# Kernel optimization log

Hardware: AMD Instinct MI355X
Metric: run time of the kernel (lower is better)

## Reference

```python
import jax, jax.numpy as jnp
import numpy as np

DRN = 0.4
TWO_PI = 2.0 * np.pi


def _mlp(x, ws, bs):
    # torch_geometric MLP with act='LeakyRelu' (slope 0.01), dropout=0 (eval), norm treated as identity (eval running stats)
    for w, b in zip(ws[:-1], bs[:-1]):
        x = jax.nn.leaky_relu(x @ w + b, 0.01)
    return x @ ws[-1] + bs[-1]


def _conv(x, ws, bs):
    # x: [B, N, F] = [pt, h..., ang_re, ang_im]. Dense masked equivalent of radius-graph EdgeConv.
    ang = x[..., -2:]
    d2 = jnp.sum((ang[:, :, None, :] - ang[:, None, :, :]) ** 2, -1)
    adj = (d2 <= DRN * DRN).astype(x.dtype)  # [B,N,N], i=target, j=source, self-loops included (radius ball)
    h = x[..., 1:-2]
    B, N, H = h.shape
    hi = jnp.broadcast_to(h[:, :, None, :], (B, N, N, H))
    hj = jnp.broadcast_to(h[:, None, :, :], (B, N, N, H))
    re, im = ang[..., 0], ang[..., 1]
    r2 = re * re + im * im
    nrm = jnp.maximum(jnp.sqrt(r2[:, :, None] * r2[:, None, :]), 1e-12)
    cos = (re[:, :, None] * re[:, None, :] + im[:, :, None] * im[:, None, :]) / nrm
    sin = (im[:, :, None] * re[:, None, :] - re[:, :, None] * im[:, None, :]) / nrm
    feat = jnp.concatenate([hi, hj, hj - hi, cos[..., None], sin[..., None]], -1)
    m = _mlp(feat, ws, bs)  # [B,N,N,H_out+1]
    # pt-weighted aggregation: message pt is the TARGET's pt (x_i[:, :1] in torch code)
    pt = x[..., 0]
    msg_pt = pt[:, :, None] * adj
    denom = jnp.sum(msg_pt, -1, keepdims=True)
    w = jnp.where(denom > 0, msg_pt / denom, 0.0)  # nan_to_num equivalent
    agg = jnp.einsum('bij,bijk->bik', w, m)
    sw = jnp.sum(w, -1)
    agg_pt = pt * sw                      # sum_j w * pt_i
    agg_ang = ang * sw[..., None]          # sum_j w * ang_i
    # phase renormalization: exp(2*pi*i*gamma) * (re + i*im)
    gamma = agg[..., -1]
    c, s = jnp.cos(TWO_PI * gamma), jnp.sin(TWO_PI * gamma)
    re2 = c * agg_ang[..., 0] - s * agg_ang[..., 1]
    im2 = s * agg_ang[..., 0] + c * agg_ang[..., 1]
    return jnp.concatenate([agg_pt[..., None], agg[..., :-1], re2[..., None], im2[..., None]], -1)


def _forward(pt, angles, c0w, c0b, c1w, c1b, rw, rb):
    absz = jnp.sqrt(jnp.sum(angles ** 2, -1))  # |view_as_complex(angles)|
    x = jnp.concatenate([pt[..., None], absz[..., None], angles], -1)
    x = _conv(x, c0w, c0b)
    x = _conv(x, c1w, c1b)
    # pt-weighted readout over particles
    ptf = x[..., 0]
    denom = jnp.sum(ptf, -1, keepdims=True)
    wj = jnp.where(denom > 0, ptf / denom, 0.0)
    xg = jnp.einsum('bn,bnf->bf', wj, x[..., 1:])
    logits = _mlp(xg[:, :-2], rw, rb)
    return jnp.concatenate([jax.nn.sigmoid(logits), xg[:, -2:]], -1)


def setup_inputs() -> dict:
    key = jax.random.key(0)
    ks = jax.random.split(key, 16)
    B, N = 128, 128
    pt = jax.random.uniform(ks[0], (B, N), jnp.float32, 0.05, 1.0)  # all > 0 so mask is all-true
    angles = 0.25 * jax.random.normal(ks[1], (B, N, 2), jnp.float32)

    def lin(k, i, o):
        return (0.2 / np.sqrt(i)) * jax.random.normal(k, (i, o), jnp.float32) * np.sqrt(i)

    H = 16
    return {
        'pt': pt, 'angles': angles,
        'c0_w0': lin(ks[2], 5, H), 'c0_b0': jnp.zeros((H,), jnp.float32),
        'c0_w1': lin(ks[3], H, H + 1), 'c0_b1': jnp.zeros((H + 1,), jnp.float32),
        'c1_w0': lin(ks[4], 3 * H + 2, H), 'c1_b0': jnp.zeros((H,), jnp.float32),
        'c1_w1': lin(ks[5], H, H + 1), 'c1_b1': jnp.zeros((H + 1,), jnp.float32),
        'r_w0': lin(ks[6], H, 32), 'r_b0': jnp.zeros((32,), jnp.float32),
        'r_w1': lin(ks[7], 32, 32), 'r_b1': jnp.zeros((32,), jnp.float32),
        'r_w2': lin(ks[8], 32, 1), 'r_b2': jnp.zeros((1,), jnp.float32),
    }


def reference(pt, angles, c0_w0, c0_b0, c0_w1, c0_b1, c1_w0, c1_b0, c1_w1, c1_b1, r_w0, r_b0, r_w1, r_b1, r_w2, r_b2):
    return _forward(pt, angles, (c0_w0, c0_w1), (c0_b0, c0_b1), (c1_w0, c1_w1), (c1_b0, c1_b1), (r_w0, r_w1, r_w2), (r_b0, r_b1, r_b2))
```

## Files before the change

### kernel.cpp

```cpp
#include <hip/hip_runtime.h>
#include <math.h>


#define BB 128
#define NN 128
#define BN (BB * NN)

typedef float f32x2 __attribute__((ext_vector_type(2)));

__device__ __forceinline__ f32x2 pk2(float s) { f32x2 r; r[0] = s; r[1] = s; return r; }
__device__ __forceinline__ f32x2 pkfma(f32x2 a, f32x2 b, f32x2 c) {
    return __builtin_elementwise_fma(a, b, c);
}
__device__ __forceinline__ f32x2 pkmax(f32x2 a, f32x2 b) {
    return __builtin_elementwise_max(a, b);
}

template <int CTRL>
__device__ __forceinline__ float dpp_add(float x) {
    int t = __builtin_amdgcn_update_dpp(0, __float_as_int(x), CTRL, 0xF, 0xF, true);
    return x + __int_as_float(t);
}

__device__ __forceinline__ float wave_sum64(float x) {
    x = dpp_add<0xB1>(x);
    x = dpp_add<0x4E>(x);
    x = dpp_add<0x114>(x);
    x = dpp_add<0x118>(x);
    x = dpp_add<0x142>(x);
    x = dpp_add<0x143>(x);
    return __int_as_float(__builtin_amdgcn_readlane(__float_as_int(x), 63));
}

template <int L>
__global__ __launch_bounds__(256) void conv_kernel(
    const float* __restrict__ ang,
    const float* __restrict__ u,
    const float* __restrict__ v,
    const float* __restrict__ w0,
    const float* __restrict__ b0,
    const float* __restrict__ w1,
    const float* __restrict__ b1,
    const float* __restrict__ nw0,
    const float* __restrict__ nb0,
    float* __restrict__ out_u,
    float* __restrict__ out_v,
    float* __restrict__ out_ang,
    float* __restrict__ y)
{
    const int lane = threadIdx.x & 63;
    const int wid  = threadIdx.x >> 6;
    const int ni   = __builtin_amdgcn_readfirstlane(blockIdx.x * 4 + wid);
    const int base = ni & ~(NN - 1);

    const float2 aiv = ((const float2*)ang)[ni];
    const float rei = aiv.x, imi = aiv.y;
    const float r2i = fmaf(rei, rei, imi * imi);

    constexpr int cosrow = (L == 0) ? 3 : 48;

    f32x2 u0b2[8], q02[8], wc2[8], ws2[8];
    if constexpr (L == 0) {
        const float abszi = __builtin_amdgcn_sqrtf(r2i);
        #pragma unroll
        for (int p = 0; p < 8; ++p) {
            f32x2 wa = *(const f32x2*)(w0 + 2 * p);
            f32x2 wb = *(const f32x2*)(w0 + 16 + 2 * p);
            f32x2 wcv = *(const f32x2*)(w0 + 32 + 2 * p);
            f32x2 bb = *(const f32x2*)(b0 + 2 * p);
            u0b2[p] = pkfma(pk2(abszi), wa - wcv, bb);
            q02[p]  = wb + wcv;
            wc2[p]  = *(const f32x2*)(w0 + cosrow * 16 + 2 * p);
            ws2[p]  = *(const f32x2*)(w0 + (cosrow + 1) * 16 + 2 * p);
        }
    } else {
        #pragma unroll
        for (int p = 0; p < 8; ++p) {
            f32x2 uu; uu[0] = u[ni * 16 + 2 * p]; uu[1] = u[ni * 16 + 2 * p + 1];
            u0b2[p] = uu;
            wc2[p]  = *(const f32x2*)(w0 + cosrow * 16 + 2 * p);
            ws2[p]  = *(const f32x2*)(w0 + (cosrow + 1) * 16 + 2 * p);
        }
    }

    f32x2 A2[8];
    #pragma unroll
    for (int p = 0; p < 8; ++p) A2[p] = pk2(0.0f);
    int deg = 0;

    #pragma unroll
    for (int jj = 0; jj < 2; ++jj) {
        const int nj = base + lane + jj * 64;
        const float2 ajv = ((const float2*)ang)[nj];
        const float rej = ajv.x, imj = ajv.y;

        const float dre = rei - rej, dim = imi - imj;
        const float d2 = fmaf(dre, dre, dim * dim);
        const bool isadj = (d2 <= 0.16f);
        deg += (int)__popcll(__ballot(isadj));
        const f32x2 adj2 = pk2(isadj ? 1.0f : 0.0f);

        const float r2j = fmaf(rej, rej, imj * imj);
        const float inv = fminf(rsqrtf(r2i * r2j), 1e12f);
        const f32x2 cos2 = pk2(fmaf(rei, rej, imi * imj) * inv);
        const f32x2 sin2 = pk2(fmaf(imi, rej, -(rei * imj)) * inv);

        f32x2 vj2[8];
        f32x2 ab2;
        if constexpr (L == 0) {
            ab2 = pk2(__builtin_amdgcn_sqrtf(r2j));
        } else {
            const float4* vp = (const float4*)(v + (size_t)nj * 16);
            float4 a0 = vp[0], a1 = vp[1], a2 = vp[2], a3 = vp[3];
            vj2[0][0] = a0.x; vj2[0][1] = a0.y; vj2[1][0] = a0.z; vj2[1][1] = a0.w;
            vj2[2][0] = a1.x; vj2[2][1] = a1.y; vj2[3][0] = a1.z; vj2[3][1] = a1.w;
            vj2[4][0] = a2.x; vj2[4][1] = a2.y; vj2[5][0] = a2.z; vj2[5][1] = a2.w;
            vj2[6][0] = a3.x; vj2[6][1] = a3.y; vj2[7][0] = a3.z; vj2[7][1] = a3.w;
        }

        #pragma unroll
        for (int p = 0; p < 8; ++p) {
            f32x2 z;
            if constexpr (L == 0) z = pkfma(ab2, q02[p], u0b2[p]);
            else                  z = u0b2[p] + vj2[p];
            z = pkfma(cos2, wc2[p], z);
            z = pkfma(sin2, ws2[p], z);
            f32x2 a = pkmax(z, z * 0.01f);
            A2[p] = pkfma(a, adj2, A2[p]);
        }
    }

    float Ak[16];
    #pragma unroll
    for (int p = 0; p < 8; ++p) {
        Ak[2 * p]     = wave_sum64(A2[p][0]);
        Ak[2 * p + 1] = wave_sum64(A2[p][1]);
    }
    const float invdeg = __builtin_amdgcn_rcpf((float)deg);

    float aggv = 0.0f;
    if (lane < 17) {
        float s = 0.0f;
        #pragma unroll
        for (int k = 0; k < 16; ++k) s = fmaf(Ak[k], w1[k * 17 + lane], s);
        aggv = fmaf(s, invdeg, b1[lane]);
    }

    __shared__ float h1s[4][16];

    if constexpr (L == 0) {
        if (lane < 16) h1s[wid][lane] = aggv;
        if (lane == 16) {
            float g = aggv - floorf(aggv);
            float cs = __builtin_amdgcn_cosf(g);
            float sn = __builtin_amdgcn_sinf(g);
            float re2 = cs * rei - sn * imi;
            float im2 = fmaf(sn, rei, cs * imi);
            ((float2*)out_ang)[ni] = make_float2(re2, im2);
        }
        __syncthreads();
        if (lane < 32) {
            const int k = lane & 15;
            const bool isU = lane < 16;
            const int off = isU ? 0 : 256;
            const float sgn = isU ? -1.0f : 1.0f;
            float acc = isU ? nb0[k] : 0.0f;
            #pragma unroll
            for (int c = 0; c < 16; ++c) {
                float wa  = nw0[off + c * 16 + k];
                float wcv = nw0[512 + c * 16 + k];
                acc = fmaf(h1s[wid][c], fmaf(sgn, wcv, wa), acc);
            }
            if (isU) out_u[ni * 16 + k] = acc;
            else     out_v[ni * 16 + k] = acc;
        }
    } else {
        if (lane < 16) y[ni * 18 + lane] = aggv;
        if (lane == 16) {
            float g = aggv - floorf(aggv);
            float cs = __builtin_amdgcn_cosf(g);
            float sn = __builtin_amdgcn_sinf(g);
            y[ni * 18 + 16] = cs * rei - sn * imi;
            y[ni * 18 + 17] = fmaf(sn, rei, cs * imi);
        }
    }
}

__global__ __launch_bounds__(128) void readout_kernel(
    const float* __restrict__ pt,
    const float* __restrict__ y,
    const float* __restrict__ w0, const float* __restrict__ b0,
    const float* __restrict__ w1, const float* __restrict__ b1,
    const float* __restrict__ w2, const float* __restrict__ b2,
    float* __restrict__ out) {
    int b = blockIdx.x;
    int tid = threadIdx.x;
    int n = b * NN + tid;
    float ptf = pt[n];
    const float* yn = y + (size_t)n * 18;

    __shared__ float sred[2][18];
    __shared__ float xg[18];
    __shared__ float h1s[32];

    float tot = ptf;
#pragma unroll
    for (int off = 32; off; off >>= 1) tot += __shfl_xor(tot, off);
    if ((tid & 63) == 0) sred[tid >> 6][0] = tot;
    __syncthreads();
    float denom = sred[0][0] + sred[1][0];
    float wj = (denom > 0.0f) ? (ptf / denom) : 0.0f;
    __syncthreads();

    float vals[18];
#pragma unroll
    for (int f = 0; f < 18; ++f) vals[f] = wj * yn[f];
#pragma unroll
    for (int f = 0; f < 18; ++f) {
        float s = vals[f];
#pragma unroll
        for (int off = 32; off; off >>= 1) s += __shfl_xor(s, off);
        vals[f] = s;
    }
    if ((tid & 63) == 0) {
#pragma unroll
        for (int f = 0; f < 18; ++f) sred[tid >> 6][f] = vals[f];
    }
    __syncthreads();
    if (tid < 18) xg[tid] = sred[0][tid] + sred[1][tid];
    __syncthreads();

    if (tid < 32) {
        float h = b0[tid];
#pragma unroll
        for (int k = 0; k < 16; ++k) h = fmaf(xg[k], w0[k * 32 + tid], h);
        h = fmaxf(h, 0.01f * h);
        h1s[tid] = h;
    }
    __syncthreads();
    if (tid < 32) {
        float h = b1[tid];
#pragma unroll
        for (int k = 0; k < 32; ++k) h = fmaf(h1s[k], w1[k * 32 + tid], h);
        h = fmaxf(h, 0.01f * h);
        float p = h * w2[tid];
#pragma unroll
        for (int off = 16; off; off >>= 1) p += __shfl_xor(p, off, 32);
        if (tid == 0) {
            out[b * 3 + 0] = 1.0f / (1.0f + expf(-(p + b2[0])));
            out[b * 3 + 1] = xg[16];
            out[b * 3 + 2] = xg[17];
        }
    }
}

extern "C" void kernel_launch(void* const* d_in, const int* in_sizes, int n_in,
                              void* d_out, int out_size, void* d_ws, size_t ws_size,
                              hipStream_t stream) {
    const float* pt    = (const float*)d_in[0];
    const float* ang   = (const float*)d_in[1];
    const float* c0_w0 = (const float*)d_in[2];
    const float* c0_b0 = (const float*)d_in[3];
    const float* c0_w1 = (const float*)d_in[4];
    const float* c0_b1 = (const float*)d_in[5];
    const float* c1_w0 = (const float*)d_in[6];
    const float* c1_b0 = (const float*)d_in[7];
    const float* c1_w1 = (const float*)d_in[8];
    const float* c1_b1 = (const float*)d_in[9];
    const float* r_w0  = (const float*)d_in[10];
    const float* r_b0  = (const float*)d_in[11];
    const float* r_w1  = (const float*)d_in[12];
    const float* r_b1  = (const float*)d_in[13];
    const float* r_w2  = (const float*)d_in[14];
    const float* r_b2  = (const float*)d_in[15];
    float* out = (float*)d_out;
    float* ws = (float*)d_ws;

    float* ang1 = ws;
    float* u1   = ang1 + (size_t)BN * 2;
    float* v1   = u1 + (size_t)BN * 16;
    float* y1   = v1 + (size_t)BN * 16;

    hipLaunchKernelGGL((conv_kernel<0>), dim3(BN / 4), dim3(256), 0, stream,
                       ang, (const float*)nullptr, (const float*)nullptr,
                       c0_w0, c0_b0, c0_w1, c0_b1,
                       c1_w0, c1_b0, u1, v1, ang1, (float*)nullptr);
    hipLaunchKernelGGL((conv_kernel<1>), dim3(BN / 4), dim3(256), 0, stream,
                       ang1, u1, v1,
                       c1_w0, (const float*)nullptr, c1_w1, c1_b1,
                       (const float*)nullptr, (const float*)nullptr,
                       (float*)nullptr, (float*)nullptr, (float*)nullptr, y1);
    hipLaunchKernelGGL(readout_kernel, dim3(BB), dim3(128), 0, stream,
                       pt, y1, r_w0, r_b0, r_w1, r_b1, r_w2, r_b2, out);
}
```

Measured before the change: 35.12 us.

## Map four nodes per wave with 16-lane groups and fuse pooling into conv1

Each wave now handles four target nodes, with each 16-lane group looping over all 128 sources, instead of one node per wave using two iterations. Group-local DPP sums plus a bpermute broadcast replace the full 64-lane reductions. Every lane computes its own output feature and gamma, which removes the lane<17 serial tail. Layer-2 pt-weighted pooling is partially reduced inside conv1 and written as per-wave partials, so readout only sums 32 partials instead of rereading the full feature tensor. The per-node inverse norm is cached in ang1 for reuse, at the cost of more registers and a longer per-lane loop.

```diff
diff --git a/kernel.cpp b/kernel.cpp
--- a/kernel.cpp
+++ b/kernel.cpp
@@ -18,111 +18,108 @@
 
 template <int CTRL>
 __device__ __forceinline__ float dpp_add(float x) {
-    int t = __builtin_amdgcn_update_dpp(0, __float_as_int(x), CTRL, 0xF, 0xF, true);
-    return x + __int_as_float(t);
-}
-
-__device__ __forceinline__ float wave_sum64(float x) {
+    int tmp = __builtin_amdgcn_update_dpp(0, __float_as_int(x), CTRL, 0xF, 0xF, true);
+    return x + __int_as_float(tmp);
+}
+
+__device__ __forceinline__ float grp16_sum(float x) {
     x = dpp_add<0xB1>(x);
     x = dpp_add<0x4E>(x);
     x = dpp_add<0x114>(x);
     x = dpp_add<0x118>(x);
-    x = dpp_add<0x142>(x);
-    x = dpp_add<0x143>(x);
-    return __int_as_float(__builtin_amdgcn_readlane(__float_as_int(x), 63));
-}
-
-template <int L>
-__global__ __launch_bounds__(256) void conv_kernel(
+    return x;
+}
+
+__device__ __forceinline__ float bcast_grp(float x, int bidx) {
+    return __int_as_float(__builtin_amdgcn_ds_bpermute(bidx, __float_as_int(x)));
+}
+
+__global__ __launch_bounds__(256) void conv0_kernel(
     const float* __restrict__ ang,
-    const float* __restrict__ u,
-    const float* __restrict__ v,
     const float* __restrict__ w0,
     const float* __restrict__ b0,
     const float* __restrict__ w1,
     const float* __restrict__ b1,
     const float* __restrict__ nw0,
     const float* __restrict__ nb0,
-    float* __restrict__ out_u,
-    float* __restrict__ out_v,
-    float* __restrict__ out_ang,
-    float* __restrict__ y)
+    float* __restrict__ ang1,
+    float* __restrict__ u1,
+    float* __restrict__ v1)
 {
-    const int lane = threadIdx.x & 63;
-    const int wid  = threadIdx.x >> 6;
-    const int ni   = __builtin_amdgcn_readfirstlane(blockIdx.x * 4 + wid);
-    const int base = ni & ~(NN - 1);
-
-    const float2 aiv = ((const float2*)ang)[ni];
-    const float rei = aiv.x, imi = aiv.y;
-    const float r2i = fmaf(rei, rei, imi * imi);
-
-    constexpr int cosrow = (L == 0) ? 3 : 48;
+    const int tid  = threadIdx.x;
+    const int lane = tid & 63;
+    const int wid  = tid >> 6;
+    const int t    = lane & 15;
+    const int g    = lane >> 4;
+    const int ni   = blockIdx.x * 16 + wid * 4 + g;
+    const int base = (blockIdx.x >> 3) << 7;
+
+    __shared__ float hls[16][17];
+
+    const float2 ai = ((const float2*)ang)[ni];
+    const float r2i = fmaf(ai.x, ai.x, ai.y * ai.y);
+    const float abszi = __builtin_amdgcn_sqrtf(r2i);
+    const float invi  = __builtin_amdgcn_rsqf(r2i);
 
     f32x2 u0b2[8], q02[8], wc2[8], ws2[8];
-    if constexpr (L == 0) {
-        const float abszi = __builtin_amdgcn_sqrtf(r2i);
+    #pragma unroll
+    for (int p = 0; p < 8; ++p) {
+        f32x2 wa  = *(const f32x2*)(w0 + 2 * p);
+        f32x2 wb  = *(const f32x2*)(w0 + 16 + 2 * p);
+        f32x2 wcv = *(const f32x2*)(w0 + 32 + 2 * p);
+        f32x2 bb  = *(const f32x2*)(b0 + 2 * p);
+        u0b2[p] = pkfma(pk2(abszi), wa - wcv, bb);
+        q02[p]  = wb + wcv;
+        wc2[p]  = *(const f32x2*)(w0 + 48 + 2 * p);
+        ws2[p]  = *(const f32x2*)(w0 + 64 + 2 * p);
+    }
+
+    float w1row[16], w1g[16];
+    #pragma unroll
+    for (int k = 0; k < 16; ++k) {
+        w1row[k] = w1[k * 17 + t];
+        w1g[k]   = w1[k * 17 + 16];
+    }
+    const float b1t = b1[t], b1g = b1[16];
+
+    const int o   = lane & 31;
+    const int kk  = o & 15;
+    const bool isU = (o < 16);
+    float wk[16];
+    {
+        const int off = isU ? 0 : 256;
+        #pragma unroll
+        for (int c = 0; c < 16; ++c) {
+            float a_ = nw0[off + c * 16 + kk];
+            float c_ = nw0[512 + c * 16 + kk];
+            wk[c] = isU ? (a_ - c_) : (a_ + c_);
+        }
+    }
+    const float accb = isU ? nb0[kk] : 0.0f;
+
+    f32x2 A2[8];
+    #pragma unroll
+    for (int p = 0; p < 8; ++p) A2[p] = pk2(0.0f);
+    float degf = 0.0f;
+
+    #pragma unroll 4
+    for (int jj = 0; jj < 8; ++jj) {
+        const float2 aj = ((const float2*)ang)[base + jj * 16 + t];
+        const float r2j = fmaf(aj.x, aj.x, aj.y * aj.y);
+        const float abszj = __builtin_amdgcn_sqrtf(r2j);
+        const float ivj   = __builtin_amdgcn_rsqf(r2j);
+        const float dre = ai.x - aj.x, dim = ai.y - aj.y;
+        const float d2 = fmaf(dre, dre, dim * dim);
+        const float adjf = (d2 <= 0.16f) ? 1.0f : 0.0f;
+        degf += adjf;
+        const float inv = fminf(invi * ivj, 1e12f);
+        const f32x2 cos2 = pk2(fmaf(ai.x, aj.x, ai.y * aj.y) * inv);
+        const f32x2 sin2 = pk2(fmaf(ai.y, aj.x, -(ai.x * aj.y)) * inv);
+        const f32x2 ab2 = pk2(abszj);
+        const f32x2 adj2 = pk2(adjf);
         #pragma unroll
         for (int p = 0; p < 8; ++p) {
-            f32x2 wa = *(const f32x2*)(w0 + 2 * p);
-            f32x2 wb = *(const f32x2*)(w0 + 16 + 2 * p);
-            f32x2 wcv = *(const f32x2*)(w0 + 32 + 2 * p);
-            f32x2 bb = *(const f32x2*)(b0 + 2 * p);
-            u0b2[p] = pkfma(pk2(abszi), wa - wcv, bb);
-            q02[p]  = wb + wcv;
-            wc2[p]  = *(const f32x2*)(w0 + cosrow * 16 + 2 * p);
-            ws2[p]  = *(const f32x2*)(w0 + (cosrow + 1) * 16 + 2 * p);
-        }
-    } else {
-        #pragma unroll
-        for (int p = 0; p < 8; ++p) {
-            f32x2 uu; uu[0] = u[ni * 16 + 2 * p]; uu[1] = u[ni * 16 + 2 * p + 1];
-            u0b2[p] = uu;
-            wc2[p]  = *(const f32x2*)(w0 + cosrow * 16 + 2 * p);
-            ws2[p]  = *(const f32x2*)(w0 + (cosrow + 1) * 16 + 2 * p);
-        }
-    }
-
-    f32x2 A2[8];
-    #pragma unroll
-    for (int p = 0; p < 8; ++p) A2[p] = pk2(0.0f);
-    int deg = 0;
-
-    #pragma unroll
-    for (int jj = 0; jj < 2; ++jj) {
-        const int nj = base + lane + jj * 64;
-        const float2 ajv = ((const float2*)ang)[nj];
-        const float rej = ajv.x, imj = ajv.y;
-
-        const float dre = rei - rej, dim = imi - imj;
-        const float d2 = fmaf(dre, dre, dim * dim);
-        const bool isadj = (d2 <= 0.16f);
-        deg += (int)__popcll(__ballot(isadj));
-        const f32x2 adj2 = pk2(isadj ? 1.0f : 0.0f);
-
-        const float r2j = fmaf(rej, rej, imj * imj);
-        const float inv = fminf(rsqrtf(r2i * r2j), 1e12f);
-        const f32x2 cos2 = pk2(fmaf(rei, rej, imi * imj) * inv);
-        const f32x2 sin2 = pk2(fmaf(imi, rej, -(rei * imj)) * inv);
-
-        f32x2 vj2[8];
-        f32x2 ab2;
-        if constexpr (L == 0) {
-            ab2 = pk2(__builtin_amdgcn_sqrtf(r2j));
-        } else {
-            const float4* vp = (const float4*)(v + (size_t)nj * 16);
-            float4 a0 = vp[0], a1 = vp[1], a2 = vp[2], a3 = vp[3];
-            vj2[0][0] = a0.x; vj2[0][1] = a0.y; vj2[1][0] = a0.z; vj2[1][1] = a0.w;
-            vj2[2][0] = a1.x; vj2[2][1] = a1.y; vj2[3][0] = a1.z; vj2[3][1] = a1.w;
-            vj2[4][0] = a2.x; vj2[4][1] = a2.y; vj2[5][0] = a2.z; vj2[5][1] = a2.w;
-            vj2[6][0] = a3.x; vj2[6][1] = a3.y; vj2[7][0] = a3.z; vj2[7][1] = a3.w;
-        }
-
-        #pragma unroll
-        for (int p = 0; p < 8; ++p) {
-            f32x2 z;
-            if constexpr (L == 0) z = pkfma(ab2, q02[p], u0b2[p]);
-            else                  z = u0b2[p] + vj2[p];
+            f32x2 z = pkfma(ab2, q02[p], u0b2[p]);
             z = pkfma(cos2, wc2[p], z);
             z = pkfma(sin2, ws2[p], z);
             f32x2 a = pkmax(z, z * 0.01f);
@@ -130,123 +127,221 @@
         }
     }
 
+    const int bidx = (lane | 15) << 2;
     float Ak[16];
     #pragma unroll
     for (int p = 0; p < 8; ++p) {
-        Ak[2 * p]     = wave_sum64(A2[p][0]);
-        Ak[2 * p + 1] = wave_sum64(A2[p][1]);
-    }
-    const float invdeg = __builtin_amdgcn_rcpf((float)deg);
-
-    float aggv = 0.0f;
-    if (lane < 17) {
-        float s = 0.0f;
-        #pragma unroll
-        for (int k = 0; k < 16; ++k) s = fmaf(Ak[k], w1[k * 17 + lane], s);
-        aggv = fmaf(s, invdeg, b1[lane]);
-    }
-
-    __shared__ float h1s[4][16];
-
-    if constexpr (L == 0) {
-        if (lane < 16) h1s[wid][lane] = aggv;
-        if (lane == 16) {
-            float g = aggv - floorf(aggv);
-            float cs = __builtin_amdgcn_cosf(g);
-            float sn = __builtin_amdgcn_sinf(g);
-            float re2 = cs * rei - sn * imi;
-            float im2 = fmaf(sn, rei, cs * imi);
-            ((float2*)out_ang)[ni] = make_float2(re2, im2);
-        }
-        __syncthreads();
-        if (lane < 32) {
-            const int k = lane & 15;
-            const bool isU = lane < 16;
-            const int off = isU ? 0 : 256;
-            const float sgn = isU ? -1.0f : 1.0f;
-            float acc = isU ? nb0[k] : 0.0f;
-            #pragma unroll
-            for (int c = 0; c < 16; ++c) {
-                float wa  = nw0[off + c * 16 + k];
-                float wcv = nw0[512 + c * 16 + k];
-                acc = fmaf(h1s[wid][c], fmaf(sgn, wcv, wa), acc);
-            }
-            if (isU) out_u[ni * 16 + k] = acc;
-            else     out_v[ni * 16 + k] = acc;
-        }
-    } else {
-        if (lane < 16) y[ni * 18 + lane] = aggv;
-        if (lane == 16) {
-            float g = aggv - floorf(aggv);
-            float cs = __builtin_amdgcn_cosf(g);
-            float sn = __builtin_amdgcn_sinf(g);
-            y[ni * 18 + 16] = cs * rei - sn * imi;
-            y[ni * 18 + 17] = fmaf(sn, rei, cs * imi);
-        }
-    }
-}
-
-__global__ __launch_bounds__(128) void readout_kernel(
+        Ak[2 * p]     = bcast_grp(grp16_sum(A2[p][0]), bidx);
+        Ak[2 * p + 1] = bcast_grp(grp16_sum(A2[p][1]), bidx);
+    }
+    const float degA = bcast_grp(grp16_sum(degf), bidx);
+    const float invdeg = __builtin_amdgcn_rcpf(degA);
+
+    float s = 0.0f, sg = 0.0f;
+    #pragma unroll
+    for (int k = 0; k < 16; ++k) {
+        s  = fmaf(Ak[k], w1row[k], s);
+        sg = fmaf(Ak[k], w1g[k], sg);
+    }
+    const float mt    = fmaf(s, invdeg, b1t);
+    const float gamma = fmaf(sg, invdeg, b1g);
+
+    {
+        const float gf = gamma - floorf(gamma);
+        const float cs = __builtin_amdgcn_cosf(gf);
+        const float sn = __builtin_amdgcn_sinf(gf);
+        const float re2 = cs * ai.x - sn * ai.y;
+        const float im2 = fmaf(sn, ai.x, cs * ai.y);
+        if (t == 0) ((float4*)ang1)[ni] = make_float4(re2, im2, invi, 0.0f);
+    }
+
+    hls[wid * 4 + g][t] = mt;
+
+    #pragma unroll
+    for (int p = 0; p < 2; ++p) {
+        const int nl = (lane >> 5) + 2 * p;
+        const int node = wid * 4 + nl;
+        float acc = accb;
+        #pragma unroll
+        for (int c = 0; c < 16; ++c) acc = fmaf(hls[node][c], wk[c], acc);
+        const int nig = blockIdx.x * 16 + nl;
+        const int nout = (blockIdx.x * 16 + node);
+        (void)nig;
+        if (isU) u1[nout * 16 + kk] = acc;
+        else     v1[nout * 16 + kk] = acc;
+    }
+}
+
+__global__ __launch_bounds__(256) void conv1_kernel(
     const float* __restrict__ pt,
-    const float* __restrict__ y,
+    const float* __restrict__ ang1,
+    const float* __restrict__ u1,
+    const float* __restrict__ v1,
+    const float* __restrict__ w0,
+    const float* __restrict__ w1,
+    const float* __restrict__ b1,
+    float* __restrict__ part)
+{
+    const int tid  = threadIdx.x;
+    const int lane = tid & 63;
+    const int wid  = tid >> 6;
+    const int t    = lane & 15;
+    const int g    = lane >> 4;
+    const int ni   = blockIdx.x * 16 + wid * 4 + g;
+    const int base = (blockIdx.x >> 3) << 7;
+
+    const float4 a4 = ((const float4*)ang1)[ni];
+    const float rei = a4.x, imi = a4.y, invi = a4.z;
+    const float ptf = pt[ni];
+
+    f32x2 u0b2[8], wc2[8], ws2[8];
+    {
+        const float4* ug = (const float4*)(u1 + (size_t)ni * 16);
+        float4 q0 = ug[0], q1 = ug[1], q2 = ug[2], q3 = ug[3];
+        u0b2[0][0] = q0.x; u0b2[0][1] = q0.y; u0b2[1][0] = q0.z; u0b2[1][1] = q0.w;
+        u0b2[2][0] = q1.x; u0b2[2][1] = q1.y; u0b2[3][0] = q1.z; u0b2[3][1] = q1.w;
+        u0b2[4][0] = q2.x; u0b2[4][1] = q2.y; u0b2[5][0] = q2.z; u0b2[5][1] = q2.w;
+        u0b2[6][0] = q3.x; u0b2[6][1] = q3.y; u0b2[7][0] = q3.z; u0b2[7][1] = q3.w;
+    }
+    #pragma unroll
+    for (int p = 0; p < 8; ++p) {
+        wc2[p] = *(const f32x2*)(w0 + 768 + 2 * p);
+        ws2[p] = *(const f32x2*)(w0 + 784 + 2 * p);
+    }
+
+    float w1row[16], w1g[16];
+    #pragma unroll
+    for (int k = 0; k < 16; ++k) {
+        w1row[k] = w1[k * 17 + t];
+        w1g[k]   = w1[k * 17 + 16];
+    }
+    const float b1t = b1[t], b1g = b1[16];
+
+    f32x2 A2[8];
+    #pragma unroll
+    for (int p = 0; p < 8; ++p) A2[p] = pk2(0.0f);
+    float degf = 0.0f;
+
+    #pragma unroll 4
+    for (int jj = 0; jj < 8; ++jj) {
+        const int j = base + jj * 16 + t;
+        const float4 aj = ((const float4*)ang1)[j];
+        f32x2 vj2[8];
+        {
+            const float4* vg = (const float4*)(v1 + (size_t)j * 16);
+            float4 q0 = vg[0], q1 = vg[1], q2 = vg[2], q3 = vg[3];
+            vj2[0][0] = q0.x; vj2[0][1] = q0.y; vj2[1][0] = q0.z; vj2[1][1] = q0.w;
+            vj2[2][0] = q1.x; vj2[2][1] = q1.y; vj2[3][0] = q1.z; vj2[3][1] = q1.w;
+            vj2[4][0] = q2.x; vj2[4][1] = q2.y; vj2[5][0] = q2.z; vj2[5][1] = q2.w;
+            vj2[6][0] = q3.x; vj2[6][1] = q3.y; vj2[7][0] = q3.z; vj2[7][1] = q3.w;
+        }
+        const float dre = rei - aj.x, dim = imi - aj.y;
+        const float d2 = fmaf(dre, dre, dim * dim);
+        const float adjf = (d2 <= 0.16f) ? 1.0f : 0.0f;
+        degf += adjf;
+        const float inv = fminf(invi * aj.z, 1e12f);
+        const f32x2 cos2 = pk2(fmaf(rei, aj.x, imi * aj.y) * inv);
+        const f32x2 sin2 = pk2(fmaf(imi, aj.x, -(rei * aj.y)) * inv);
+        const f32x2 adj2 = pk2(adjf);
+        #pragma unroll
+        for (int p = 0; p < 8; ++p) {
+            f32x2 z = u0b2[p] + vj2[p];
+            z = pkfma(cos2, wc2[p], z);
+            z = pkfma(sin2, ws2[p], z);
+            f32x2 a = pkmax(z, z * 0.01f);
+            A2[p] = pkfma(a, adj2, A2[p]);
+        }
+    }
+
+    const int bidx = (lane | 15) << 2;
+    float Ak[16];
+    #pragma unroll
+    for (int p = 0; p < 8; ++p) {
+        Ak[2 * p]     = bcast_grp(grp16_sum(A2[p][0]), bidx);
+        Ak[2 * p + 1] = bcast_grp(grp16_sum(A2[p][1]), bidx);
+    }
+    const float degA = bcast_grp(grp16_sum(degf), bidx);
+    const float invdeg = __builtin_amdgcn_rcpf(degA);
+
+    float s = 0.0f, sg = 0.0f;
+    #pragma unroll
+    for (int k = 0; k < 16; ++k) {
+        s  = fmaf(Ak[k], w1row[k], s);
+        sg = fmaf(Ak[k], w1g[k], sg);
+    }
+    const float mt    = fmaf(s, invdeg, b1t);
+    const float gamma = fmaf(sg, invdeg, b1g);
+
+    const float gf = gamma - floorf(gamma);
+    const float cs = __builtin_amdgcn_cosf(gf);
+    const float sn = __builtin_amdgcn_sinf(gf);
+    const float re2 = cs * rei - sn * imi;
+    const float im2 = fmaf(sn, rei, cs * imi);
+
+    float pm  = ptf * mt;
+    float pre = ptf * re2;
+    float pim = ptf * im2;
+    float ppt = ptf;
+    pm  += __int_as_float(__builtin_amdgcn_ds_swizzle(__float_as_int(pm),  0x401F));
+    pre += __int_as_float(__builtin_amdgcn_ds_swizzle(__float_as_int(pre), 0x401F));
+    pim += __int_as_float(__builtin_amdgcn_ds_swizzle(__float_as_int(pim), 0x401F));
+    ppt += __int_as_float(__builtin_amdgcn_ds_swizzle(__float_as_int(ppt), 0x401F));
+    pm  += __shfl_xor(pm, 32);
+    pre += __shfl_xor(pre, 32);
+    pim += __shfl_xor(pim, 32);
+    ppt += __shfl_xor(ppt, 32);
+
+    float* po = part + (size_t)(blockIdx.x * 4 + wid) * 20;
+    if (lane < 16)       po[lane] = pm;
+    else if (lane == 16) po[16] = pre;
+    else if (lane == 17) po[17] = pim;
+    else if (lane == 18) po[18] = ppt;
+}
+
+__global__ __launch_bounds__(64) void readout_kernel(
+    const float* __restrict__ part,
     const float* __restrict__ w0, const float* __restrict__ b0,
     const float* __restrict__ w1, const float* __restrict__ b1,
     const float* __restrict__ w2, const float* __restrict__ b2,
     float* __restrict__ out) {
-    int b = blockIdx.x;
-    int tid = threadIdx.x;
-    int n = b * NN + tid;
-    float ptf = pt[n];
-    const float* yn = y + (size_t)n * 18;
-
-    __shared__ float sred[2][18];
+    const int b = blockIdx.x;
+    const int t = threadIdx.x;
+
+    __shared__ float sbuf[19];
     __shared__ float xg[18];
-    __shared__ float h1s[32];
-
-    float tot = ptf;
-#pragma unroll
-    for (int off = 32; off; off >>= 1) tot += __shfl_xor(tot, off);
-    if ((tid & 63) == 0) sred[tid >> 6][0] = tot;
-    __syncthreads();
-    float denom = sred[0][0] + sred[1][0];
-    float wj = (denom > 0.0f) ? (ptf / denom) : 0.0f;
-    __syncthreads();
-
-    float vals[18];
-#pragma unroll
-    for (int f = 0; f < 18; ++f) vals[f] = wj * yn[f];
-#pragma unroll
-    for (int f = 0; f < 18; ++f) {
-        float s = vals[f];
-#pragma unroll
-        for (int off = 32; off; off >>= 1) s += __shfl_xor(s, off);
-        vals[f] = s;
-    }
-    if ((tid & 63) == 0) {
-#pragma unroll
-        for (int f = 0; f < 18; ++f) sred[tid >> 6][f] = vals[f];
-    }
-    __syncthreads();
-    if (tid < 18) xg[tid] = sred[0][tid] + sred[1][tid];
-    __syncthreads();
-
-    if (tid < 32) {
-        float h = b0[tid];
-#pragma unroll
-        for (int k = 0; k < 16; ++k) h = fmaf(xg[k], w0[k * 32 + tid], h);
+    __shared__ float h1r[32];
+
+    if (t < 19) {
+        float s0 = 0.0f, s1 = 0.0f, s2 = 0.0f, s3 = 0.0f;
+        const float* pb = part + (size_t)b * 32 * 20 + t;
+        #pragma unroll
+        for (int r = 0; r < 32; r += 4) {
+            s0 += pb[(r + 0) * 20];
+            s1 += pb[(r + 1) * 20];
+            s2 += pb[(r + 2) * 20];
+            s3 += pb[(r + 3) * 20];
+        }
+        sbuf[t] = (s0 + s1) + (s2 + s3);
+    }
+    const float invd = __builtin_amdgcn_rcpf(sbuf[18]);
+    if (t < 18) xg[t] = sbuf[t] * invd;
+
+    if (t < 32) {
+        float h = b0[t];
+        #pragma unroll
+        for (int k = 0; k < 16; ++k) h = fmaf(xg[k], w0[k * 32 + t], h);
         h = fmaxf(h, 0.01f * h);
-        h1s[tid] = h;
-    }
-    __syncthreads();
-    if (tid < 32) {
-        float h = b1[tid];
-#pragma unroll
-        for (int k = 0; k < 32; ++k) h = fmaf(h1s[k], w1[k * 32 + tid], h);
+        h1r[t] = h;
+    }
+    if (t < 32) {
+        float h = b1[t];
+        #pragma unroll
+        for (int k = 0; k < 32; ++k) h = fmaf(h1r[k], w1[k * 32 + t], h);
         h = fmaxf(h, 0.01f * h);
-        float p = h * w2[tid];
-#pragma unroll
-        for (int off = 16; off; off >>= 1) p += __shfl_xor(p, off, 32);
-        if (tid == 0) {
+        float p = h * w2[t];
+        #pragma unroll
+        for (int off = 16; off; off >>= 1) p += __shfl_xor(p, off);
+        if (t == 0) {
             out[b * 3 + 0] = 1.0f / (1.0f + expf(-(p + b2[0])));
             out[b * 3 + 1] = xg[16];
             out[b * 3 + 2] = xg[17];
@@ -276,20 +371,16 @@
     float* out = (float*)d_out;
     float* ws = (float*)d_ws;
 
-    float* ang1 = ws;
-    float* u1   = ang1 + (size_t)BN * 2;
-    float* v1   = u1 + (size_t)BN * 16;
-    float* y1   = v1 + (size_t)BN * 16;
-
-    hipLaunchKernelGGL((conv_kernel<0>), dim3(BN / 4), dim3(256), 0, stream,
-                       ang, (const float*)nullptr, (const float*)nullptr,
-                       c0_w0, c0_b0, c0_w1, c0_b1,
-                       c1_w0, c1_b0, u1, v1, ang1, (float*)nullptr);
-    hipLaunchKernelGGL((conv_kernel<1>), dim3(BN / 4), dim3(256), 0, stream,
-                       ang1, u1, v1,
-                       c1_w0, (const float*)nullptr, c1_w1, c1_b1,
-                       (const float*)nullptr, (const float*)nullptr,
-                       (float*)nullptr, (float*)nullptr, (float*)nullptr, y1);
-    hipLaunchKernelGGL(readout_kernel, dim3(BB), dim3(128), 0, stream,
-                       pt, y1, r_w0, r_b0, r_w1, r_b1, r_w2, r_b2, out);
-}
+    float* ang1  = ws;
+    float* u1    = ang1 + (size_t)BN * 4;
+    float* v1    = u1 + (size_t)BN * 16;
+    float* partb = v1 + (size_t)BN * 16;
+
+    hipLaunchKernelGGL(conv0_kernel, dim3(BN / 16), dim3(256), 0, stream,
+                       ang, c0_w0, c0_b0, c0_w1, c0_b1, c1_w0, c1_b0,
+                       ang1, u1, v1);
+    hipLaunchKernelGGL(conv1_kernel, dim3(BN / 16), dim3(256), 0, stream,
+                       pt, ang1, u1, v1, c1_w0, c1_w1, c1_b1, partb);
+    hipLaunchKernelGGL(readout_kernel, dim3(BB), dim3(64), 0, stream,
+                       partb, r_w0, r_b0, r_w1, r_b1, r_w2, r_b2, out);
+}
```

New measurement: 30.21 us. -14.0%, faster.
